# Optimization experiments

Hardware: AMD Instinct MI355X
Metric: run time of the kernel (lower is better)

## Reference

```python
import jax, jax.numpy as jnp
import numpy as np

N_NODES = 50000
N_EDGES = 800000
IN_FEATS = 128
HIDDEN = 256
N_CLASSES = 64


def setup_inputs() -> dict:
    key = jax.random.key(0)
    ks = jax.random.split(key, 16)
    def w(k, shape, fan_in):
        return jax.random.normal(k, shape, dtype=jnp.float32) * (1.0 / np.sqrt(fan_in))
    inp = {
        "x": jax.random.normal(ks[0], (N_NODES, IN_FEATS), dtype=jnp.float32),
        "edge_src": jax.random.randint(ks[1], (N_EDGES,), 0, N_NODES, dtype=jnp.int32),
        "edge_dst": jax.random.randint(ks[2], (N_EDGES,), 0, N_NODES, dtype=jnp.int32),
        # layer 0: in_feats -> hidden
        "W0s": w(ks[3], (IN_FEATS, HIDDEN), IN_FEATS),
        "W0n": w(ks[4], (IN_FEATS, HIDDEN), IN_FEATS),
        "b0": jnp.zeros((HIDDEN,), dtype=jnp.float32),
        # layer 1: hidden -> hidden
        "W1s": w(ks[5], (HIDDEN, HIDDEN), HIDDEN),
        "W1n": w(ks[6], (HIDDEN, HIDDEN), HIDDEN),
        "b1": jnp.zeros((HIDDEN,), dtype=jnp.float32),
        # layer 2: hidden -> hidden (last conv also outputs hidden per source code)
        "W2s": w(ks[7], (HIDDEN, HIDDEN), HIDDEN),
        "W2n": w(ks[8], (HIDDEN, HIDDEN), HIDDEN),
        "b2": jnp.zeros((HIDDEN,), dtype=jnp.float32),
        # fc1: hidden -> n_classes
        "Wfc": w(ks[9], (HIDDEN, N_CLASSES), HIDDEN),
        "bfc": jnp.zeros((N_CLASSES,), dtype=jnp.float32),
    }
    return inp


def _sage_layer(h, src, dst, Ws, Wn, b):
    # mean-neighbor aggregation: segment-sum messages, divide by in-degree
    msg = h[src]  # [E, D] irregular gather
    agg = jax.ops.segment_sum(msg, dst, num_segments=N_NODES)  # [N, D]
    deg = jax.ops.segment_sum(jnp.ones_like(dst, dtype=h.dtype), dst, num_segments=N_NODES)
    h_neigh = agg / jnp.maximum(deg, 1.0)[:, None]
    # DGL SAGEConv (mean): fc_self(h) + fc_neigh(h_neigh) + bias
    return h @ Ws + h_neigh @ Wn + b


def reference(x, edge_src, edge_dst, W0s, W0n, b0, W1s, W1n, b1, W2s, W2n, b2, Wfc, bfc):
    # forward applies dropout (identity at eval) and NO activation between layers,
    # matching the original module's forward().
    h = _sage_layer(x, edge_src, edge_dst, W0s, W0n, b0)
    h = _sage_layer(h, edge_src, edge_dst, W1s, W1n, b1)
    h = _sage_layer(h, edge_src, edge_dst, W2s, W2n, b2)
    return h @ Wfc + bfc  # [N, n_classes]
```

## Files before the change

kernel.cpp:

```cpp
#include <hip/hip_runtime.h>

#define NN 50000
#define NE 800000
#define F_IN 128
#define HID 256
#define N_CLS 64
#define SCAN_BLOCKS ((NN + 255) / 256)
#define CROWS 515

typedef _Float16 half8 __attribute__((ext_vector_type(8)));
typedef float f32x4 __attribute__((ext_vector_type(4)));

__global__ void hist_count(const int* __restrict__ dst, int* __restrict__ cnt,
                           unsigned short* __restrict__ rank, int E) {
    int i = blockIdx.x * blockDim.x + threadIdx.x;
    if (i < E) rank[i] = (unsigned short)atomicAdd(&cnt[dst[i]], 1);
}

__device__ __forceinline__ void scan_block_sums_dev(const int* __restrict__ cnt,
                                                    int* __restrict__ blockSums, int n) {
    __shared__ int s[256];
    int t = threadIdx.x;
    int i = blockIdx.x * 256 + t;
    s[t] = (i < n) ? cnt[i] : 0;
    __syncthreads();
    for (int off = 128; off > 0; off >>= 1) {
        if (t < off) s[t] += s[t + off];
        __syncthreads();
    }
    if (t == 0) blockSums[blockIdx.x] = s[0];
}

__device__ __forceinline__ void scan_top_dev(int* __restrict__ blockSums, int nb) {
    __shared__ int s[256];
    int t = threadIdx.x;
    s[t] = (t < nb) ? blockSums[t] : 0;
    __syncthreads();
    for (int off = 1; off < 256; off <<= 1) {
        int v = (t >= off) ? s[t - off] : 0;
        __syncthreads();
        s[t] += v;
        __syncthreads();
    }
    if (t < nb) blockSums[t] = (t > 0) ? s[t - 1] : 0;
}

__device__ __forceinline__ void scan_final_dev(const int* __restrict__ cnt,
                                               const int* __restrict__ blockBase,
                                               int* __restrict__ offs,
                                               float* __restrict__ dinv, int n) {
    __shared__ int s[256];
    int t = threadIdx.x;
    int i = blockIdx.x * 256 + t;
    int v = (i < n) ? cnt[i] : 0;
    s[t] = v;
    __syncthreads();
    for (int off = 1; off < 256; off <<= 1) {
        int u = (t >= off) ? s[t - off] : 0;
        __syncthreads();
        s[t] += u;
        __syncthreads();
    }
    if (i < n) {
        offs[i] = blockBase[blockIdx.x] + s[t] - v;
        dinv[i] = 1.0f / (float)max(v, 1);
    }
    if (i == n - 1) offs[n] = blockBase[blockIdx.x] + s[t];
}

__global__ void csr_place2(const int* __restrict__ src, const int* __restrict__ dst,
                           const unsigned short* __restrict__ rank, const int* __restrict__ offs,
                           unsigned short* __restrict__ csr, int E) {
    int e = blockIdx.x * blockDim.x + threadIdx.x;
    if (e < E) csr[offs[dst[e]] + rank[e]] = (unsigned short)src[e];
}

__device__ __forceinline__ const float* virtC1_row(int r, const float* W0s,
                                                   const float* W0n, const float* b0) {
    if (r < 0) return nullptr;
    if (r < 128) return W0s + (size_t)r * 256;
    if (r < 256) return W0n + (size_t)(r - 128) * 256;
    if (r == 512) return b0;
    return nullptr;
}

__device__ __forceinline__ int shift_src(int r) {
    if (r >= 128 && r < 512) return r - 128;
    if (r == 513) return 512;
    if (r == 514) return 513;
    return -1;
}


__device__ __forceinline__ void compose_first_dev(
    int bx, const float* __restrict__ W0s, const float* __restrict__ W0n,
    const float* __restrict__ b0,
    const float* __restrict__ B1, const float* __restrict__ B2,
    const float* __restrict__ brow, float* __restrict__ C)
{
    __shared__ float As[64][17];
    __shared__ float Bs[16][64];
    const int tid = threadIdx.x;
    const int tx = tid & 15, ty = tid >> 4;
    const int row0 = (bx % 9) * 64;
    const int col0 = (bx / 9) * 64;
    const int lr = tid >> 2, lc = tid & 3;
    const int br = tid >> 4, bc = tid & 15;

    float acc[4][4] = {};

    for (int pass = 0; pass < 2; ++pass) {
        const float* B = pass ? B2 : B1;
        int grow = row0 + lr;
        int srcr = pass ? shift_src(grow) : (grow < CROWS ? grow : -1);
        const float* ap = virtC1_row(srcr, W0s, W0n, b0);

        for (int k0 = 0; k0 < 256; k0 += 16) {
            float4 av = make_float4(0.f, 0.f, 0.f, 0.f);
            if (ap) av = *(const float4*)(ap + k0 + lc * 4);
            As[lr][lc * 4 + 0] = av.x;
            As[lr][lc * 4 + 1] = av.y;
            As[lr][lc * 4 + 2] = av.z;
            As[lr][lc * 4 + 3] = av.w;
            *(float4*)&Bs[br][bc * 4] = *(const float4*)(B + (size_t)(k0 + br) * 256 + col0 + bc * 4);
            __syncthreads();
            #pragma unroll
            for (int k = 0; k < 16; ++k) {
                float a[4];
                #pragma unroll
                for (int i = 0; i < 4; ++i) a[i] = As[ty * 4 + i][k];
                float4 bv = *(const float4*)&Bs[k][tx * 4];
                const float b[4] = {bv.x, bv.y, bv.z, bv.w};
                #pragma unroll
                for (int i = 0; i < 4; ++i)
                    #pragma unroll
                    for (int j = 0; j < 4; ++j)
                        acc[i][j] += a[i] * b[j];
            }
            __syncthreads();
        }
    }

    #pragma unroll
    for (int i = 0; i < 4; ++i) {
        int r = row0 + ty * 4 + i;
        if (r < CROWS) {
            #pragma unroll
            for (int j = 0; j < 4; ++j) {
                float v = acc[i][j];
                if (r == 512) v += brow[col0 + tx * 4 + j];
                C[(size_t)r * 256 + col0 + tx * 4 + j] = v;
            }
        }
    }
}

__device__ __forceinline__ void compose_mid_dev(
    int bx, const float* __restrict__ A,
    const float* __restrict__ B1, const float* __restrict__ B2,
    const float* __restrict__ brow, float* __restrict__ C)
{
    __shared__ float As[64][17];
    __shared__ float Bs[16][64];
    const int tid = threadIdx.x;
    const int tx = tid & 15, ty = tid >> 4;
    const int row0 = (bx % 9) * 64;
    const int col0 = (bx / 9) * 64;
    const int lr = tid >> 2, lc = tid & 3;
    const int br = tid >> 4, bc = tid & 15;

    float acc[4][4] = {};

    for (int pass = 0; pass < 2; ++pass) {
        const float* B = pass ? B2 : B1;
        int grow = row0 + lr;
        int p = pass ? shift_src(grow) : (grow < CROWS ? grow : -1);

        for (int k0 = 0; k0 < 256; k0 += 16) {
            float4 av = make_float4(0.f, 0.f, 0.f, 0.f);
            if (p >= 0) av = *(const float4*)(A + (size_t)p * 256 + k0 + lc * 4);
            As[lr][lc * 4 + 0] = av.x;
            As[lr][lc * 4 + 1] = av.y;
            As[lr][lc * 4 + 2] = av.z;
            As[lr][lc * 4 + 3] = av.w;
            *(float4*)&Bs[br][bc * 4] = *(const float4*)(B + (size_t)(k0 + br) * 256 + col0 + bc * 4);
            __syncthreads();
            #pragma unroll
            for (int k = 0; k < 16; ++k) {
                float a[4];
                #pragma unroll
                for (int i = 0; i < 4; ++i) a[i] = As[ty * 4 + i][k];
                float4 bv = *(const float4*)&Bs[k][tx * 4];
                const float b[4] = {bv.x, bv.y, bv.z, bv.w};
                #pragma unroll
                for (int i = 0; i < 4; ++i)
                    #pragma unroll
                    for (int j = 0; j < 4; ++j)
                        acc[i][j] += a[i] * b[j];
            }
            __syncthreads();
        }
    }

    #pragma unroll
    for (int i = 0; i < 4; ++i) {
        int r = row0 + ty * 4 + i;
        if (r < CROWS) {
            #pragma unroll
            for (int j = 0; j < 4; ++j) {
                float v = acc[i][j];
                if (r == 512) v += brow[col0 + tx * 4 + j];
                C[(size_t)r * 256 + col0 + tx * 4 + j] = v;
            }
        }
    }
}

__device__ __forceinline__ void compose_last_dev(
    int bx, const float* __restrict__ A, const float* __restrict__ B1,
    const float* __restrict__ brow, float* __restrict__ Vf, _Float16* __restrict__ BT)
{
    __shared__ float As[64][17];
    __shared__ float Bs[16][64];
    const int tid = threadIdx.x;
    const int tx = tid & 15, ty = tid >> 4;
    const int row0 = bx * 64;
    const int lr = tid >> 2, lc = tid & 3;
    const int br = tid >> 4, bc = tid & 15;

    float acc[4][4] = {};

    for (int k0 = 0; k0 < 256; k0 += 16) {
        float4 av = make_float4(0.f, 0.f, 0.f, 0.f);
        int grow = row0 + lr;
        if (grow < CROWS) av = *(const float4*)(A + (size_t)grow * 256 + k0 + lc * 4);
        As[lr][lc * 4 + 0] = av.x;
        As[lr][lc * 4 + 1] = av.y;
        As[lr][lc * 4 + 2] = av.z;
        As[lr][lc * 4 + 3] = av.w;
        *(float4*)&Bs[br][bc * 4] = *(const float4*)(B1 + (size_t)(k0 + br) * 64 + bc * 4);
        __syncthreads();
        #pragma unroll
        for (int k = 0; k < 16; ++k) {
            float a[4];
            #pragma unroll
            for (int i = 0; i < 4; ++i) a[i] = As[ty * 4 + i][k];
            float4 bv = *(const float4*)&Bs[k][tx * 4];
            const float b[4] = {bv.x, bv.y, bv.z, bv.w};
            #pragma unroll
            for (int i = 0; i < 4; ++i)
                #pragma unroll
                for (int j = 0; j < 4; ++j)
                    acc[i][j] += a[i] * b[j];
        }
        __syncthreads();
    }

    #pragma unroll
    for (int i = 0; i < 4; ++i) {
        int r = row0 + ty * 4 + i;
        if (r < CROWS) {
            #pragma unroll
            for (int j = 0; j < 4; ++j) {
                int c = tx * 4 + j;
                float v = acc[i][j];
                if (r == 512) v += brow[c];
                Vf[(size_t)r * 64 + c] = v;
                if (r < 512)
                    BT[(size_t)((r >> 7) * 64 + c) * 128 + (r & 127)] = (_Float16)v;
            }
        }
    }
}

__global__ __launch_bounds__(256) void k_scanA_composeF(
    const int* __restrict__ cnt, int* __restrict__ blockSums,
    const float* __restrict__ W0s, const float* __restrict__ W0n, const float* __restrict__ b0,
    const float* __restrict__ W1s, const float* __restrict__ W1n, const float* __restrict__ b1,
    float* __restrict__ C2)
{
    if (blockIdx.x < SCAN_BLOCKS) scan_block_sums_dev(cnt, blockSums, NN);
    else compose_first_dev(blockIdx.x - SCAN_BLOCKS, W0s, W0n, b0, W1s, W1n, b1, C2);
}

__global__ __launch_bounds__(256) void k_scanT_composeM(
    int* __restrict__ blockSums,
    const float* __restrict__ C2,
    const float* __restrict__ W2s, const float* __restrict__ W2n, const float* __restrict__ b2,
    float* __restrict__ C3)
{
    if (blockIdx.x == 0) scan_top_dev(blockSums, SCAN_BLOCKS);
    else compose_mid_dev(blockIdx.x - 1, C2, W2s, W2n, b2, C3);
}

__global__ __launch_bounds__(256) void k_scanF_composeL(
    const int* __restrict__ cnt, const int* __restrict__ blockBase,
    int* __restrict__ offs, float* __restrict__ dinv,
    const float* __restrict__ C3, const float* __restrict__ Wfc, const float* __restrict__ bfc,
    float* __restrict__ Vf, _Float16* __restrict__ BT)
{
    if (blockIdx.x < SCAN_BLOCKS) scan_final_dev(cnt, blockBase, offs, dinv, NN);
    else compose_last_dev(blockIdx.x - SCAN_BLOCKS, C3, Wfc, bfc, Vf, BT);
}

__global__ __launch_bounds__(256) void gemm_Y(
    const float* __restrict__ X, const _Float16* __restrict__ BT,
    _Float16* __restrict__ Y, _Float16* __restrict__ Tc, int N)
{
    constexpr int LP = 40;
    __shared__ _Float16 As[128 * LP];
    __shared__ _Float16 Bs[128 * LP];

    const int tid = threadIdx.x;
    const int wave = tid >> 6;
    const int lane = tid & 63;
    const int l15 = lane & 15;
    const int quad = lane >> 4;
    const int wrow = wave >> 1;
    const int wcol = wave & 1;
    const int m_base = wrow * 64;
    const int n_base = wcol * 64;

    const int row0 = blockIdx.x * 128;
    const int col0 = blockIdx.y * 128;

    f32x4 acc[4][4] = {};

    for (int k0 = 0; k0 < 128; k0 += 32) {
        #pragma unroll
        for (int r = 0; r < 2; ++r) {
            int idx = r * 256 + tid;
            int row = idx >> 2, ch = idx & 3;
            int gr = row0 + row; if (gr > N - 1) gr = N - 1;
            const float* ap = X + (size_t)gr * 128 + k0 + ch * 8;
            float4 f0 = *(const float4*)ap;
            float4 f1 = *(const float4*)(ap + 4);
            half8 v = { (_Float16)f0.x, (_Float16)f0.y, (_Float16)f0.z, (_Float16)f0.w,
                        (_Float16)f1.x, (_Float16)f1.y, (_Float16)f1.z, (_Float16)f1.w };
            *(half8*)&As[row * LP + ch * 8] = v;
        }
        #pragma unroll
        for (int r = 0; r < 2; ++r) {
            int idx = r * 256 + tid;
            int row = idx >> 2, ch = idx & 3;
            *(half8*)&Bs[row * LP + ch * 8] =
                *(const half8*)(BT + (size_t)(col0 + row) * 128 + k0 + ch * 8);
        }
        __syncthreads();
        half8 af[4], bf[4];
        #pragma unroll
        for (int i = 0; i < 4; ++i)
            af[i] = *(const half8*)&As[(m_base + i * 16 + l15) * LP + quad * 8];
        #pragma unroll
        for (int j = 0; j < 4; ++j)
            bf[j] = *(const half8*)&Bs[(n_base + j * 16 + l15) * LP + quad * 8];
        #pragma unroll
        for (int i = 0; i < 4; ++i)
            #pragma unroll
            for (int j = 0; j < 4; ++j)
                acc[i][j] = __builtin_amdgcn_mfma_f32_16x16x32_f16(af[i], bf[j], acc[i][j], 0, 0, 0);
        __syncthreads();
    }

    #pragma unroll
    for (int i = 0; i < 4; ++i) {
        #pragma unroll
        for (int j = 0; j < 4; ++j) {
            int col = col0 + n_base + j * 16 + l15;
            #pragma unroll
            for (int r = 0; r < 4; ++r) {
                int row = row0 + m_base + i * 16 + quad * 4 + r;
                if (row < N) {
                    _Float16 v = (_Float16)acc[i][j][r];
                    Y[(size_t)row * 256 + col] = v;
                    if (col >= 192) Tc[(size_t)row * 64 + (col - 192)] = v;
                }
            }
        }
    }
}

template <bool OUT_F32>
__global__ __launch_bounds__(256) void gather64(
    const _Float16* __restrict__ Tin,
    const unsigned short* __restrict__ csr, const int* __restrict__ offs,
    const float* __restrict__ dinv,
    const _Float16* __restrict__ Yadd,
    const float* __restrict__ cvec,
    void* __restrict__ Tout, int N)
{
    int node = blockIdx.x * 32 + (threadIdx.x >> 3);
    int lane = threadIdx.x & 7;
    if (node >= N) return;
    int beg = offs[node], end = offs[node + 1];
    float acc[8] = {};
    int e = beg;
    for (; e + 3 < end; e += 4) {
        int s0 = csr[e], s1 = csr[e + 1], s2 = csr[e + 2], s3 = csr[e + 3];
        half8 v0 = *(const half8*)(Tin + (size_t)s0 * 64 + lane * 8);
        half8 v1 = *(const half8*)(Tin + (size_t)s1 * 64 + lane * 8);
        half8 v2 = *(const half8*)(Tin + (size_t)s2 * 64 + lane * 8);
        half8 v3 = *(const half8*)(Tin + (size_t)s3 * 64 + lane * 8);
        #pragma unroll
        for (int j = 0; j < 8; ++j)
            acc[j] += ((float)v0[j] + (float)v1[j]) + ((float)v2[j] + (float)v3[j]);
    }
    for (; e < end; ++e) {
        half8 v = *(const half8*)(Tin + (size_t)csr[e] * 64 + lane * 8);
        #pragma unroll
        for (int j = 0; j < 8; ++j) acc[j] += (float)v[j];
    }
    float sc = dinv[node];
    half8 y = *(const half8*)(Yadd + (size_t)node * 256 + lane * 8);
    if (OUT_F32) {
        float* o = (float*)Tout + (size_t)node * 64 + lane * 8;
        float4 o0, o1;
        o0.x = acc[0] * sc + (float)y[0] + cvec[lane * 8 + 0];
        o0.y = acc[1] * sc + (float)y[1] + cvec[lane * 8 + 1];
        o0.z = acc[2] * sc + (float)y[2] + cvec[lane * 8 + 2];
        o0.w = acc[3] * sc + (float)y[3] + cvec[lane * 8 + 3];
        o1.x = acc[4] * sc + (float)y[4] + cvec[lane * 8 + 4];
        o1.y = acc[5] * sc + (float)y[5] + cvec[lane * 8 + 5];
        o1.z = acc[6] * sc + (float)y[6] + cvec[lane * 8 + 6];
        o1.w = acc[7] * sc + (float)y[7] + cvec[lane * 8 + 7];
        *(float4*)o = o0;
        *(float4*)(o + 4) = o1;
    } else {
        half8 o;
        #pragma unroll
        for (int j = 0; j < 8; ++j)
            o[j] = (_Float16)(acc[j] * sc + (float)y[j] + cvec[lane * 8 + j]);
        *(half8*)((_Float16*)Tout + (size_t)node * 64 + lane * 8) = o;
    }
}

extern "C" void kernel_launch(void* const* d_in, const int* in_sizes, int n_in,
                              void* d_out, int out_size, void* d_ws, size_t ws_size,
                              hipStream_t stream) {
    const float* x    = (const float*)d_in[0];
    const int*   esrc = (const int*)d_in[1];
    const int*   edst = (const int*)d_in[2];
    const float* W0s  = (const float*)d_in[3];
    const float* W0n  = (const float*)d_in[4];
    const float* b0   = (const float*)d_in[5];
    const float* W1s  = (const float*)d_in[6];
    const float* W1n  = (const float*)d_in[7];
    const float* b1   = (const float*)d_in[8];
    const float* W2s  = (const float*)d_in[9];
    const float* W2n  = (const float*)d_in[10];
    const float* b2   = (const float*)d_in[11];
    const float* Wfc  = (const float*)d_in[12];
    const float* bfc  = (const float*)d_in[13];
    float* out = (float*)d_out;

    _Float16* Y   = (_Float16*)d_ws;
    _Float16* Ta  = Y + (size_t)NN * 256;
    _Float16* Tb  = Ta + (size_t)NN * 64;
    _Float16* Tc  = Tb + (size_t)NN * 64;
    _Float16* BT  = Tc + (size_t)NN * 64;
    float* C2     = (float*)(BT + 256 * 128);
    float* C3     = C2 + CROWS * 256;
    float* Vf     = C3 + CROWS * 256;
    float* dinv   = Vf + CROWS * 64;
    int* cnt      = (int*)(dinv + NN);
    int* offs     = cnt + NN;
    int* blockSums = offs + NN + 1;
    unsigned short* rank = (unsigned short*)(blockSums + SCAN_BLOCKS);
    unsigned short* csr  = rank + NE;

    hipMemsetAsync(cnt, 0, (size_t)NN * sizeof(int), stream);
    hist_count<<<(NE + 255) / 256, 256, 0, stream>>>(edst, cnt, rank, NE);
    k_scanA_composeF<<<SCAN_BLOCKS + 36, 256, 0, stream>>>(
        cnt, blockSums, W0s, W0n, b0, W1s, W1n, b1, C2);
    k_scanT_composeM<<<1 + 36, 256, 0, stream>>>(blockSums, C2, W2s, W2n, b2, C3);
    k_scanF_composeL<<<SCAN_BLOCKS + 9, 256, 0, stream>>>(
        cnt, blockSums, offs, dinv, C3, Wfc, bfc, Vf, BT);
    csr_place2<<<(NE + 255) / 256, 256, 0, stream>>>(esrc, edst, rank, offs, csr, NE);

    gemm_Y<<<dim3((NN + 127) / 128, 2), 256, 0, stream>>>(x, BT, Y, Tc, NN);

    const int ggrid = (NN + 31) / 32;
    gather64<false><<<ggrid, 256, 0, stream>>>(
        Tc, csr, offs, dinv, Y + 128, Vf + (size_t)514 * 64, Ta, NN);
    gather64<false><<<ggrid, 256, 0, stream>>>(
        Ta, csr, offs, dinv, Y + 64, Vf + (size_t)513 * 64, Tb, NN);
    gather64<true><<<ggrid, 256, 0, stream>>>(
        Tb, csr, offs, dinv, Y, Vf + (size_t)512 * 64, out, NN);
}
```

Baseline: 291.3 us.

## Repack kernel pipeline, split Y into per-block planes, fold bias into GEMM

Kernel pairings are reshuffled: the edge histogram is fused with the first weight composition, and the scan stages with the later compositions. The final scan moves into the Y GEMM launch, which saves one launch. The GEMM now writes Y as four contiguous [N,64] planes with the per-layer constant vectors already added, so the gathers read compact rows and skip the cvec loads. The gather also gets an 8-wide unrolled inner loop to keep more loads in flight, at the cost of more registers.

```diff
diff --git a/kernel.cpp b/kernel.cpp
--- a/kernel.cpp
+++ b/kernel.cpp
@@ -11,24 +11,25 @@
 typedef _Float16 half8 __attribute__((ext_vector_type(8)));
 typedef float f32x4 __attribute__((ext_vector_type(4)));
 
-__global__ void hist_count(const int* __restrict__ dst, int* __restrict__ cnt,
-                           unsigned short* __restrict__ rank, int E) {
-    int i = blockIdx.x * blockDim.x + threadIdx.x;
+__device__ __forceinline__ void hist_dev(int bidx, const int* __restrict__ dst,
+                                         int* __restrict__ cnt,
+                                         unsigned short* __restrict__ rank, int E) {
+    int i = bidx * 256 + threadIdx.x;
     if (i < E) rank[i] = (unsigned short)atomicAdd(&cnt[dst[i]], 1);
 }
 
-__device__ __forceinline__ void scan_block_sums_dev(const int* __restrict__ cnt,
+__device__ __forceinline__ void scan_block_sums_dev(int bidx, const int* __restrict__ cnt,
                                                     int* __restrict__ blockSums, int n) {
     __shared__ int s[256];
     int t = threadIdx.x;
-    int i = blockIdx.x * 256 + t;
+    int i = bidx * 256 + t;
     s[t] = (i < n) ? cnt[i] : 0;
     __syncthreads();
     for (int off = 128; off > 0; off >>= 1) {
         if (t < off) s[t] += s[t + off];
         __syncthreads();
     }
-    if (t == 0) blockSums[blockIdx.x] = s[0];
+    if (t == 0) blockSums[bidx] = s[0];
 }
 
 __device__ __forceinline__ void scan_top_dev(int* __restrict__ blockSums, int nb) {
@@ -45,13 +46,13 @@
     if (t < nb) blockSums[t] = (t > 0) ? s[t - 1] : 0;
 }
 
-__device__ __forceinline__ void scan_final_dev(const int* __restrict__ cnt,
+__device__ __forceinline__ void scan_final_dev(int bidx, const int* __restrict__ cnt,
                                                const int* __restrict__ blockBase,
                                                int* __restrict__ offs,
                                                float* __restrict__ dinv, int n) {
     __shared__ int s[256];
     int t = threadIdx.x;
-    int i = blockIdx.x * 256 + t;
+    int i = bidx * 256 + t;
     int v = (i < n) ? cnt[i] : 0;
     s[t] = v;
     __syncthreads();
@@ -62,10 +63,10 @@
         __syncthreads();
     }
     if (i < n) {
-        offs[i] = blockBase[blockIdx.x] + s[t] - v;
+        offs[i] = blockBase[bidx] + s[t] - v;
         dinv[i] = 1.0f / (float)max(v, 1);
     }
-    if (i == n - 1) offs[n] = blockBase[blockIdx.x] + s[t];
+    if (i == n - 1) offs[n] = blockBase[bidx] + s[t];
 }
 
 __global__ void csr_place2(const int* __restrict__ src, const int* __restrict__ dst,
@@ -90,7 +91,6 @@
     if (r == 514) return 513;
     return -1;
 }
-
 
 __device__ __forceinline__ void compose_first_dev(
     int bx, const float* __restrict__ W0s, const float* __restrict__ W0n,
@@ -273,39 +273,10 @@
     }
 }
 
-__global__ __launch_bounds__(256) void k_scanA_composeF(
-    const int* __restrict__ cnt, int* __restrict__ blockSums,
-    const float* __restrict__ W0s, const float* __restrict__ W0n, const float* __restrict__ b0,
-    const float* __restrict__ W1s, const float* __restrict__ W1n, const float* __restrict__ b1,
-    float* __restrict__ C2)
-{
-    if (blockIdx.x < SCAN_BLOCKS) scan_block_sums_dev(cnt, blockSums, NN);
-    else compose_first_dev(blockIdx.x - SCAN_BLOCKS, W0s, W0n, b0, W1s, W1n, b1, C2);
-}
-
-__global__ __launch_bounds__(256) void k_scanT_composeM(
-    int* __restrict__ blockSums,
-    const float* __restrict__ C2,
-    const float* __restrict__ W2s, const float* __restrict__ W2n, const float* __restrict__ b2,
-    float* __restrict__ C3)
-{
-    if (blockIdx.x == 0) scan_top_dev(blockSums, SCAN_BLOCKS);
-    else compose_mid_dev(blockIdx.x - 1, C2, W2s, W2n, b2, C3);
-}
-
-__global__ __launch_bounds__(256) void k_scanF_composeL(
-    const int* __restrict__ cnt, const int* __restrict__ blockBase,
-    int* __restrict__ offs, float* __restrict__ dinv,
-    const float* __restrict__ C3, const float* __restrict__ Wfc, const float* __restrict__ bfc,
-    float* __restrict__ Vf, _Float16* __restrict__ BT)
-{
-    if (blockIdx.x < SCAN_BLOCKS) scan_final_dev(cnt, blockBase, offs, dinv, NN);
-    else compose_last_dev(blockIdx.x - SCAN_BLOCKS, C3, Wfc, bfc, Vf, BT);
-}
-
-__global__ __launch_bounds__(256) void gemm_Y(
+__device__ __forceinline__ void gemm_Y_dev(
+    int xb, int yb,
     const float* __restrict__ X, const _Float16* __restrict__ BT,
-    _Float16* __restrict__ Y, _Float16* __restrict__ Tc, int N)
+    const float* __restrict__ Vf, _Float16* __restrict__ Yd, int N)
 {
     constexpr int LP = 40;
     __shared__ _Float16 As[128 * LP];
@@ -321,8 +292,8 @@
     const int m_base = wrow * 64;
     const int n_base = wcol * 64;
 
-    const int row0 = blockIdx.x * 128;
-    const int col0 = blockIdx.y * 128;
+    const int row0 = xb * 128;
+    const int col0 = yb * 128;
 
     f32x4 acc[4][4] = {};
 
@@ -367,17 +338,55 @@
         #pragma unroll
         for (int j = 0; j < 4; ++j) {
             int col = col0 + n_base + j * 16 + l15;
+            int kb = col >> 6, c = col & 63;
+            float cadd = (kb < 3) ? Vf[(size_t)(512 + kb) * 64 + c] : 0.0f;
             #pragma unroll
             for (int r = 0; r < 4; ++r) {
                 int row = row0 + m_base + i * 16 + quad * 4 + r;
-                if (row < N) {
-                    _Float16 v = (_Float16)acc[i][j][r];
-                    Y[(size_t)row * 256 + col] = v;
-                    if (col >= 192) Tc[(size_t)row * 64 + (col - 192)] = v;
-                }
+                if (row < N)
+                    Yd[((size_t)kb * N + row) * 64 + c] = (_Float16)(acc[i][j][r] + cadd);
             }
         }
     }
+}
+
+__global__ __launch_bounds__(256) void k_composeF_hist(
+    const float* __restrict__ W0s, const float* __restrict__ W0n, const float* __restrict__ b0,
+    const float* __restrict__ W1s, const float* __restrict__ W1n, const float* __restrict__ b1,
+    float* __restrict__ C2,
+    const int* __restrict__ edst, int* __restrict__ cnt, unsigned short* __restrict__ rank)
+{
+    if (blockIdx.x < 36) compose_first_dev(blockIdx.x, W0s, W0n, b0, W1s, W1n, b1, C2);
+    else hist_dev(blockIdx.x - 36, edst, cnt, rank, NE);
+}
+
+__global__ __launch_bounds__(256) void k_composeM_scanA(
+    const float* __restrict__ C2,
+    const float* __restrict__ W2s, const float* __restrict__ W2n, const float* __restrict__ b2,
+    float* __restrict__ C3,
+    const int* __restrict__ cnt, int* __restrict__ blockSums)
+{
+    if (blockIdx.x < 36) compose_mid_dev(blockIdx.x, C2, W2s, W2n, b2, C3);
+    else scan_block_sums_dev(blockIdx.x - 36, cnt, blockSums, NN);
+}
+
+__global__ __launch_bounds__(256) void k_composeL_scanT(
+    const float* __restrict__ C3, const float* __restrict__ Wfc, const float* __restrict__ bfc,
+    float* __restrict__ Vf, _Float16* __restrict__ BT,
+    int* __restrict__ blockSums)
+{
+    if (blockIdx.x < 9) compose_last_dev(blockIdx.x, C3, Wfc, bfc, Vf, BT);
+    else scan_top_dev(blockSums, SCAN_BLOCKS);
+}
+
+__global__ __launch_bounds__(256) void k_gemmY_scanF(
+    const float* __restrict__ X, const _Float16* __restrict__ BT,
+    const float* __restrict__ Vf, _Float16* __restrict__ Yd,
+    const int* __restrict__ cnt, const int* __restrict__ blockBase,
+    int* __restrict__ offs, float* __restrict__ dinv)
+{
+    if (blockIdx.x < 782) gemm_Y_dev(blockIdx.x % 391, blockIdx.x / 391, X, BT, Vf, Yd, NN);
+    else scan_final_dev(blockIdx.x - 782, cnt, blockBase, offs, dinv, NN);
 }
 
 template <bool OUT_F32>
@@ -386,7 +395,6 @@
     const unsigned short* __restrict__ csr, const int* __restrict__ offs,
     const float* __restrict__ dinv,
     const _Float16* __restrict__ Yadd,
-    const float* __restrict__ cvec,
     void* __restrict__ Tout, int N)
 {
     int node = blockIdx.x * 32 + (threadIdx.x >> 3);
@@ -395,12 +403,21 @@
     int beg = offs[node], end = offs[node + 1];
     float acc[8] = {};
     int e = beg;
+    for (; e + 7 < end; e += 8) {
+        half8 v[8];
+        #pragma unroll
+        for (int u = 0; u < 8; ++u)
+            v[u] = *(const half8*)(Tin + (size_t)csr[e + u] * 64 + lane * 8);
+        #pragma unroll
+        for (int u = 0; u < 8; ++u)
+            #pragma unroll
+            for (int j = 0; j < 8; ++j) acc[j] += (float)v[u][j];
+    }
     for (; e + 3 < end; e += 4) {
-        int s0 = csr[e], s1 = csr[e + 1], s2 = csr[e + 2], s3 = csr[e + 3];
-        half8 v0 = *(const half8*)(Tin + (size_t)s0 * 64 + lane * 8);
-        half8 v1 = *(const half8*)(Tin + (size_t)s1 * 64 + lane * 8);
-        half8 v2 = *(const half8*)(Tin + (size_t)s2 * 64 + lane * 8);
-        half8 v3 = *(const half8*)(Tin + (size_t)s3 * 64 + lane * 8);
+        half8 v0 = *(const half8*)(Tin + (size_t)csr[e + 0] * 64 + lane * 8);
+        half8 v1 = *(const half8*)(Tin + (size_t)csr[e + 1] * 64 + lane * 8);
+        half8 v2 = *(const half8*)(Tin + (size_t)csr[e + 2] * 64 + lane * 8);
+        half8 v3 = *(const half8*)(Tin + (size_t)csr[e + 3] * 64 + lane * 8);
         #pragma unroll
         for (int j = 0; j < 8; ++j)
             acc[j] += ((float)v0[j] + (float)v1[j]) + ((float)v2[j] + (float)v3[j]);
@@ -411,25 +428,25 @@
         for (int j = 0; j < 8; ++j) acc[j] += (float)v[j];
     }
     float sc = dinv[node];
-    half8 y = *(const half8*)(Yadd + (size_t)node * 256 + lane * 8);
+    half8 y = *(const half8*)(Yadd + (size_t)node * 64 + lane * 8);
     if (OUT_F32) {
         float* o = (float*)Tout + (size_t)node * 64 + lane * 8;
         float4 o0, o1;
-        o0.x = acc[0] * sc + (float)y[0] + cvec[lane * 8 + 0];
-        o0.y = acc[1] * sc + (float)y[1] + cvec[lane * 8 + 1];
-        o0.z = acc[2] * sc + (float)y[2] + cvec[lane * 8 + 2];
-        o0.w = acc[3] * sc + (float)y[3] + cvec[lane * 8 + 3];
-        o1.x = acc[4] * sc + (float)y[4] + cvec[lane * 8 + 4];
-        o1.y = acc[5] * sc + (float)y[5] + cvec[lane * 8 + 5];
-        o1.z = acc[6] * sc + (float)y[6] + cvec[lane * 8 + 6];
-        o1.w = acc[7] * sc + (float)y[7] + cvec[lane * 8 + 7];
+        o0.x = acc[0] * sc + (float)y[0];
+        o0.y = acc[1] * sc + (float)y[1];
+        o0.z = acc[2] * sc + (float)y[2];
+        o0.w = acc[3] * sc + (float)y[3];
+        o1.x = acc[4] * sc + (float)y[4];
+        o1.y = acc[5] * sc + (float)y[5];
+        o1.z = acc[6] * sc + (float)y[6];
+        o1.w = acc[7] * sc + (float)y[7];
         *(float4*)o = o0;
         *(float4*)(o + 4) = o1;
     } else {
         half8 o;
         #pragma unroll
         for (int j = 0; j < 8; ++j)
-            o[j] = (_Float16)(acc[j] * sc + (float)y[j] + cvec[lane * 8 + j]);
+            o[j] = (_Float16)(acc[j] * sc + (float)y[j]);
         *(half8*)((_Float16*)Tout + (size_t)node * 64 + lane * 8) = o;
     }
 }
@@ -453,11 +470,10 @@
     const float* bfc  = (const float*)d_in[13];
     float* out = (float*)d_out;
 
-    _Float16* Y   = (_Float16*)d_ws;
-    _Float16* Ta  = Y + (size_t)NN * 256;
+    _Float16* Yd  = (_Float16*)d_ws;
+    _Float16* Ta  = Yd + (size_t)4 * NN * 64;
     _Float16* Tb  = Ta + (size_t)NN * 64;
-    _Float16* Tc  = Tb + (size_t)NN * 64;
-    _Float16* BT  = Tc + (size_t)NN * 64;
+    _Float16* BT  = Tb + (size_t)NN * 64;
     float* C2     = (float*)(BT + 256 * 128);
     float* C3     = C2 + CROWS * 256;
     float* Vf     = C3 + CROWS * 256;
@@ -469,21 +485,22 @@
     unsigned short* csr  = rank + NE;
 
     hipMemsetAsync(cnt, 0, (size_t)NN * sizeof(int), stream);
-    hist_count<<<(NE + 255) / 256, 256, 0, stream>>>(edst, cnt, rank, NE);
-    k_scanA_composeF<<<SCAN_BLOCKS + 36, 256, 0, stream>>>(
-        cnt, blockSums, W0s, W0n, b0, W1s, W1n, b1, C2);
-    k_scanT_composeM<<<1 + 36, 256, 0, stream>>>(blockSums, C2, W2s, W2n, b2, C3);
-    k_scanF_composeL<<<SCAN_BLOCKS + 9, 256, 0, stream>>>(
-        cnt, blockSums, offs, dinv, C3, Wfc, bfc, Vf, BT);
+
+    k_composeF_hist<<<36 + (NE + 255) / 256, 256, 0, stream>>>(
+        W0s, W0n, b0, W1s, W1n, b1, C2, edst, cnt, rank);
+    k_composeM_scanA<<<36 + SCAN_BLOCKS, 256, 0, stream>>>(
+        C2, W2s, W2n, b2, C3, cnt, blockSums);
+    k_composeL_scanT<<<9 + 1, 256, 0, stream>>>(
+        C3, Wfc, bfc, Vf, BT, blockSums);
+    k_gemmY_scanF<<<782 + SCAN_BLOCKS, 256, 0, stream>>>(
+        x, BT, Vf, Yd, cnt, blockSums, offs, dinv);
     csr_place2<<<(NE + 255) / 256, 256, 0, stream>>>(esrc, edst, rank, offs, csr, NE);
-
-    gemm_Y<<<dim3((NN + 127) / 128, 2), 256, 0, stream>>>(x, BT, Y, Tc, NN);
 
     const int ggrid = (NN + 31) / 32;
     gather64<false><<<ggrid, 256, 0, stream>>>(
-        Tc, csr, offs, dinv, Y + 128, Vf + (size_t)514 * 64, Ta, NN);
+        Yd + (size_t)3 * NN * 64, csr, offs, dinv, Yd + (size_t)2 * NN * 64, Ta, NN);
     gather64<false><<<ggrid, 256, 0, stream>>>(
-        Ta, csr, offs, dinv, Y + 64, Vf + (size_t)513 * 64, Tb, NN);
+        Ta, csr, offs, dinv, Yd + (size_t)1 * NN * 64, Tb, NN);
     gather64<true><<<ggrid, 256, 0, stream>>>(
-        Tb, csr, offs, dinv, Y, Vf + (size_t)512 * 64, out, NN);
-}
+        Tb, csr, offs, dinv, Yd, out, NN);
+}
```

Measured after the change: 296.2 us. No clear change (+1.7%).
